# Kernel optimization log

Hardware: AMD Instinct MI355X
Metric: run time of the kernel (lower is better)

Reference implementation:

```python
import jax, jax.numpy as jnp
import numpy as np

B, IN_F, OUT_F, K = 8192, 1024, 4096, 2
S = 64  # sqrt(OUT_F)


def setup_inputs() -> dict:
    key = jax.random.key(0)
    k1, k2, k3, k4 = jax.random.split(key, 4)
    x = jax.random.normal(k1, (B, IN_F), dtype=jnp.float32)
    y = jax.random.normal(k2, (B, OUT_F), dtype=jnp.float32)
    weight = jax.random.normal(k3, (OUT_F, IN_F), dtype=jnp.float32) * (1.0 / np.sqrt(IN_F))
    bias = jax.random.normal(k4, (OUT_F,), dtype=jnp.float32) * (1.0 / np.sqrt(IN_F))
    return {"x": x, "y": y, "weight": weight, "bias": bias}


def reference(x, y, weight, bias):
    # fused GEMM + bias + residual add epilogue
    out_lin = jnp.einsum('bk,nk->bn', x, weight) + bias + y  # (B, OUT_F)
    feat = out_lin.reshape(B, S, S)
    # AvgPool2d(kernel=K, stride=K)
    s_out = S // K
    pooled = feat.reshape(B, s_out, K, s_out, K).mean(axis=(2, 4))  # (B, s_out, s_out)
    # divide by global mean of the pooled map
    mean_val = pooled.mean()
    normed = pooled / mean_val
    return normed[:, None, :, :]  # (B, 1, s_out, s_out)
```

## Files before the change

### kernel.cpp

```cpp
#include <hip/hip_runtime.h>
#include <stdint.h>


#define KDIM 1024
#define NP   1024
#define BM 128
#define BN 128
#define BK 64

typedef __bf16 bf16x8 __attribute__((ext_vector_type(8)));
typedef float f32x4 __attribute__((ext_vector_type(4)));

__device__ __forceinline__ unsigned f2bf(float f) {
  union { float f; unsigned u; } v; v.f = f;
  unsigned r = v.u + 0x7fffu + ((v.u >> 16) & 1u);
  return r >> 16;
}

__device__ __forceinline__ void gload_lds16(const void* g, void* l) {
  __builtin_amdgcn_global_load_lds(
      (const __attribute__((address_space(1))) void*)g,
      (__attribute__((address_space(3))) void*)l, 16, 0, 0);
}

__global__ void k_prep(const float* __restrict__ x, const float* __restrict__ W,
                       const float* __restrict__ bias,
                       unsigned short* __restrict__ xb, unsigned short* __restrict__ wp,
                       float* __restrict__ biasp) {
  int b = blockIdx.x;
  int t = threadIdx.x;
  if (b < 4096) {
    int i = b * 256 + t;
    const float4* x4 = (const float4*)x;
    float4 a = x4[i * 2], c = x4[i * 2 + 1];
    uint4 o;
    o.x = f2bf(a.x) | (f2bf(a.y) << 16);
    o.y = f2bf(a.z) | (f2bf(a.w) << 16);
    o.z = f2bf(c.x) | (f2bf(c.y) << 16);
    o.w = f2bf(c.z) | (f2bf(c.w) << 16);
    ((uint4*)xb)[i] = o;
  } else {
    int o = b - 4096;
    int r0 = ((o >> 5) << 7) + ((o & 31) << 1);
    const float4* W4 = (const float4*)W;
    float4 w0 = W4[(r0) * 256 + t];
    float4 w1 = W4[(r0 + 1) * 256 + t];
    float4 w2 = W4[(r0 + 64) * 256 + t];
    float4 w3 = W4[(r0 + 65) * 256 + t];
    float ax = 0.25f * (w0.x + w1.x + w2.x + w3.x);
    float ay = 0.25f * (w0.y + w1.y + w2.y + w3.y);
    float az = 0.25f * (w0.z + w1.z + w2.z + w3.z);
    float aw = 0.25f * (w0.w + w1.w + w2.w + w3.w);
    uint2 pk;
    pk.x = f2bf(ax) | (f2bf(ay) << 16);
    pk.y = f2bf(az) | (f2bf(aw) << 16);
    ((uint2*)wp)[o * 256 + t] = pk;
    if (t == 0)
      biasp[o] = 0.25f * (bias[r0] + bias[r0 + 1] + bias[r0 + 64] + bias[r0 + 65]);
  }
}

__global__ __launch_bounds__(256) void k_gemm(
    const unsigned short* __restrict__ xb, const unsigned short* __restrict__ wp,
    const float* __restrict__ biasp, const float* __restrict__ y,
    float* __restrict__ out, float* __restrict__ partials) {
  __shared__ char smem[65536];

  int bid = blockIdx.x;
  int wg = (bid & 7) * 64 + (bid >> 3);
  int bm0 = (wg >> 3) * BM;
  int bn0 = (wg & 7) * BN;

  int tid = threadIdx.x;
  int lane = tid & 63;
  int wid = tid >> 6;
  int wr = wid >> 1, wc = wid & 1;

  f32x4 acc[4][4];
#pragma unroll
  for (int i = 0; i < 4; i++)
#pragma unroll
    for (int j = 0; j < 4; j++) acc[i][j] = (f32x4)0.0f;

  int srow = wid * 32 + (lane >> 3);
  int scol = (((lane & 7) ^ (lane >> 3)) << 3);
  const unsigned short* aSrc = xb + (size_t)(bm0 + srow) * KDIM + scol;
  const unsigned short* bSrc = wp + (size_t)(bn0 + srow) * KDIM + scol;
  int ldsOff = wid * 4096;

  int rbase = (lane & 15) * 128;
  int xorv = (lane & 7) << 4;
  int cb0 = (((lane >> 4) * 16)) ^ xorv;
  int cb1 = ((64 + (lane >> 4) * 16)) ^ xorv;

#define STAGE(buf, ks)                                                         \
  {                                                                            \
    int k0 = (ks) * BK;                                                        \
    char* ab = smem + (buf) * 32768 + ldsOff;                                  \
    char* bb = smem + (buf) * 32768 + 16384 + ldsOff;                          \
    _Pragma("unroll")                                                          \
    for (int i = 0; i < 4; ++i) {                                              \
      gload_lds16(aSrc + (size_t)i * 8 * KDIM + k0, ab + i * 1024);            \
      gload_lds16(bSrc + (size_t)i * 8 * KDIM + k0, bb + i * 1024);            \
    }                                                                          \
  }

  STAGE(0, 0);
  for (int ks = 0; ks < 16; ++ks) {
    int cur = ks & 1;
    if (ks < 15) {
      STAGE(cur ^ 1, ks + 1);
      asm volatile("s_waitcnt vmcnt(8)" ::: "memory");
    } else {
      asm volatile("s_waitcnt vmcnt(0)" ::: "memory");
    }
    __builtin_amdgcn_s_barrier();
    asm volatile("" ::: "memory");
    const char* Ab = smem + cur * 32768;
    const char* Bb = Ab + 16384;
#pragma unroll
    for (int kk = 0; kk < 2; ++kk) {
      int cb = kk ? cb1 : cb0;
      bf16x8 af[4], bfr[4];
#pragma unroll
      for (int mi = 0; mi < 4; ++mi)
        af[mi] = *(const bf16x8*)(Ab + (wr * 64 + mi * 16) * 128 + rbase + cb);
#pragma unroll
      for (int ni = 0; ni < 4; ++ni)
        bfr[ni] = *(const bf16x8*)(Bb + (wc * 64 + ni * 16) * 128 + rbase + cb);
#pragma unroll
      for (int mi = 0; mi < 4; ++mi)
#pragma unroll
        for (int ni = 0; ni < 4; ++ni)
          acc[mi][ni] = __builtin_amdgcn_mfma_f32_16x16x32_bf16(af[mi], bfr[ni], acc[mi][ni], 0, 0, 0);
    }
    asm volatile("" ::: "memory");
    __builtin_amdgcn_s_barrier();
  }

  const float2* y2 = (const float2*)y;
  float tsum = 0.f;
  int r_l = (lane >> 4) * 4;
  int c_l = lane & 15;
#pragma unroll
  for (int mi = 0; mi < 4; ++mi) {
#pragma unroll
    for (int ni = 0; ni < 4; ++ni) {
      int col = bn0 + wc * 64 + ni * 16 + c_l;
      float bp = biasp[col];
      int y2base = ((col >> 5) << 6) + (col & 31);
#pragma unroll
      for (int j = 0; j < 4; ++j) {
        int row = bm0 + wr * 64 + mi * 16 + r_l + j;
        float2 u = y2[(size_t)row * 2048 + y2base];
        float2 v = y2[(size_t)row * 2048 + y2base + 32];
        float val = acc[mi][ni][j] + bp + 0.25f * (u.x + u.y + v.x + v.y);
        out[(size_t)row * NP + col] = val;
        tsum += val;
      }
    }
  }
#pragma unroll
  for (int off = 32; off > 0; off >>= 1) tsum += __shfl_down(tsum, off);
  float* ws4 = (float*)smem;
  __syncthreads();
  if (lane == 0) ws4[wid] = tsum;
  __syncthreads();
  if (tid == 0) partials[bid] = ws4[0] + ws4[1] + ws4[2] + ws4[3];
}

__global__ void k_reduce(const float* __restrict__ partials, float* __restrict__ invm) {
  __shared__ float s[256];
  int t = threadIdx.x;
  s[t] = partials[t] + partials[t + 256];
  __syncthreads();
  for (int off = 128; off > 0; off >>= 1) {
    if (t < off) s[t] += s[t + off];
    __syncthreads();
  }
  if (t == 0) invm[0] = 8388608.0f / s[0];
}

__global__ void k_norm(float* __restrict__ out, const float* __restrict__ invm) {
  int i = blockIdx.x * 256 + threadIdx.x;
  float inv = invm[0];
  float4* o4 = (float4*)out;
  float4 v = o4[i];
  v.x *= inv; v.y *= inv; v.z *= inv; v.w *= inv;
  o4[i] = v;
}

extern "C" void kernel_launch(void* const* d_in, const int* in_sizes, int n_in,
                              void* d_out, int out_size, void* d_ws, size_t ws_size,
                              hipStream_t stream) {
  (void)in_sizes; (void)n_in; (void)out_size; (void)ws_size;
  const float* x = (const float*)d_in[0];
  const float* y = (const float*)d_in[1];
  const float* W = (const float*)d_in[2];
  const float* bias = (const float*)d_in[3];
  float* out = (float*)d_out;

  char* ws = (char*)d_ws;
  unsigned short* xb = (unsigned short*)(ws);
  unsigned short* wp = (unsigned short*)(ws + 16777216);
  float* biasp = (float*)(ws + 16777216 + 2097152);
  float* partials = (float*)(ws + 16777216 + 2097152 + 4096);
  float* invm = (float*)(ws + 16777216 + 2097152 + 4096 + 2048);

  hipLaunchKernelGGL(k_prep, dim3(5120), dim3(256), 0, stream, x, W, bias, xb, wp, biasp);
  hipLaunchKernelGGL(k_gemm, dim3(512), dim3(256), 0, stream, xb, wp, biasp, y, out, partials);
  hipLaunchKernelGGL(k_reduce, dim3(1), dim3(256), 0, stream, partials, invm);
  hipLaunchKernelGGL(k_norm, dim3(8192), dim3(256), 0, stream, out, invm);
}
```

Baseline: 67.75 us.

## Split A/B staging around MFMA halves, prefetch epilogue loads, fuse reduce into norm

```diff
diff --git a/kernel.cpp b/kernel.cpp
--- a/kernel.cpp
+++ b/kernel.cpp
@@ -93,24 +93,30 @@
   int cb0 = (((lane >> 4) * 16)) ^ xorv;
   int cb1 = ((64 + (lane >> 4) * 16)) ^ xorv;
 
-#define STAGE(buf, ks)                                                         \
+#define STAGE_A(buf, ks)                                                       \
   {                                                                            \
     int k0 = (ks) * BK;                                                        \
     char* ab = smem + (buf) * 32768 + ldsOff;                                  \
+    _Pragma("unroll")                                                          \
+    for (int i = 0; i < 4; ++i)                                                \
+      gload_lds16(aSrc + (size_t)i * 8 * KDIM + k0, ab + i * 1024);            \
+  }
+#define STAGE_B(buf, ks)                                                       \
+  {                                                                            \
+    int k0 = (ks) * BK;                                                        \
     char* bb = smem + (buf) * 32768 + 16384 + ldsOff;                          \
     _Pragma("unroll")                                                          \
-    for (int i = 0; i < 4; ++i) {                                              \
-      gload_lds16(aSrc + (size_t)i * 8 * KDIM + k0, ab + i * 1024);            \
+    for (int i = 0; i < 4; ++i)                                                \
       gload_lds16(bSrc + (size_t)i * 8 * KDIM + k0, bb + i * 1024);            \
-    }                                                                          \
-  }
-
-  STAGE(0, 0);
+  }
+
+  STAGE_A(0, 0);
+  STAGE_B(0, 0);
   for (int ks = 0; ks < 16; ++ks) {
     int cur = ks & 1;
     if (ks < 15) {
-      STAGE(cur ^ 1, ks + 1);
-      asm volatile("s_waitcnt vmcnt(8)" ::: "memory");
+      STAGE_A(cur ^ 1, ks + 1);
+      asm volatile("s_waitcnt vmcnt(4)" ::: "memory");
     } else {
       asm volatile("s_waitcnt vmcnt(0)" ::: "memory");
     }
@@ -118,21 +124,38 @@
     asm volatile("" ::: "memory");
     const char* Ab = smem + cur * 32768;
     const char* Bb = Ab + 16384;
-#pragma unroll
-    for (int kk = 0; kk < 2; ++kk) {
-      int cb = kk ? cb1 : cb0;
+    {
       bf16x8 af[4], bfr[4];
 #pragma unroll
       for (int mi = 0; mi < 4; ++mi)
-        af[mi] = *(const bf16x8*)(Ab + (wr * 64 + mi * 16) * 128 + rbase + cb);
+        af[mi] = *(const bf16x8*)(Ab + (wr * 64 + mi * 16) * 128 + rbase + cb0);
 #pragma unroll
       for (int ni = 0; ni < 4; ++ni)
-        bfr[ni] = *(const bf16x8*)(Bb + (wc * 64 + ni * 16) * 128 + rbase + cb);
+        bfr[ni] = *(const bf16x8*)(Bb + (wc * 64 + ni * 16) * 128 + rbase + cb0);
+      __builtin_amdgcn_s_setprio(1);
 #pragma unroll
       for (int mi = 0; mi < 4; ++mi)
 #pragma unroll
         for (int ni = 0; ni < 4; ++ni)
           acc[mi][ni] = __builtin_amdgcn_mfma_f32_16x16x32_bf16(af[mi], bfr[ni], acc[mi][ni], 0, 0, 0);
+      __builtin_amdgcn_s_setprio(0);
+    }
+    if (ks < 15) STAGE_B(cur ^ 1, ks + 1);
+    {
+      bf16x8 af[4], bfr[4];
+#pragma unroll
+      for (int mi = 0; mi < 4; ++mi)
+        af[mi] = *(const bf16x8*)(Ab + (wr * 64 + mi * 16) * 128 + rbase + cb1);
+#pragma unroll
+      for (int ni = 0; ni < 4; ++ni)
+        bfr[ni] = *(const bf16x8*)(Bb + (wc * 64 + ni * 16) * 128 + rbase + cb1);
+      __builtin_amdgcn_s_setprio(1);
+#pragma unroll
+      for (int mi = 0; mi < 4; ++mi)
+#pragma unroll
+        for (int ni = 0; ni < 4; ++ni)
+          acc[mi][ni] = __builtin_amdgcn_mfma_f32_16x16x32_bf16(af[mi], bfr[ni], acc[mi][ni], 0, 0, 0);
+      __builtin_amdgcn_s_setprio(0);
     }
     asm volatile("" ::: "memory");
     __builtin_amdgcn_s_barrier();
@@ -142,48 +165,65 @@
   float tsum = 0.f;
   int r_l = (lane >> 4) * 4;
   int c_l = lane & 15;
-#pragma unroll
-  for (int mi = 0; mi < 4; ++mi) {
-#pragma unroll
-    for (int ni = 0; ni < 4; ++ni) {
-      int col = bn0 + wc * 64 + ni * 16 + c_l;
-      float bp = biasp[col];
-      int y2base = ((col >> 5) << 6) + (col & 31);
-#pragma unroll
-      for (int j = 0; j < 4; ++j) {
-        int row = bm0 + wr * 64 + mi * 16 + r_l + j;
-        float2 u = y2[(size_t)row * 2048 + y2base];
-        float2 v = y2[(size_t)row * 2048 + y2base + 32];
-        float val = acc[mi][ni][j] + bp + 0.25f * (u.x + u.y + v.x + v.y);
-        out[(size_t)row * NP + col] = val;
-        tsum += val;
-      }
-    }
-  }
+  float2 pu[2][4], pv[2][4];
+
+#define LOADG(buf, mi, ni)                                                     \
+  {                                                                            \
+    int col = bn0 + wc * 64 + (ni) * 16 + c_l;                                 \
+    int yb = ((col >> 5) << 6) + (col & 31);                                   \
+    _Pragma("unroll")                                                          \
+    for (int j = 0; j < 4; ++j) {                                              \
+      size_t row = (size_t)(bm0 + wr * 64 + (mi) * 16 + r_l + j);              \
+      pu[buf][j] = y2[row * 2048 + yb];                                        \
+      pv[buf][j] = y2[row * 2048 + yb + 32];                                   \
+    }                                                                          \
+  }
+#define CONS(buf, mi, ni)                                                      \
+  {                                                                            \
+    int col = bn0 + wc * 64 + (ni) * 16 + c_l;                                 \
+    float bp = biasp[col];                                                     \
+    _Pragma("unroll")                                                          \
+    for (int j = 0; j < 4; ++j) {                                              \
+      int row = bm0 + wr * 64 + (mi) * 16 + r_l + j;                           \
+      float val = acc[mi][ni][j] + bp +                                        \
+                  0.25f * (pu[buf][j].x + pu[buf][j].y + pv[buf][j].x + pv[buf][j].y); \
+      out[(size_t)row * NP + col] = val;                                       \
+      tsum += val;                                                             \
+    }                                                                          \
+  }
+
+  LOADG(0, 0, 0);
+#pragma unroll
+  for (int idx = 0; idx < 16; ++idx) {
+    int mi = idx >> 2, ni = idx & 3;
+    if (idx < 15) {
+      int mi2 = (idx + 1) >> 2, ni2 = (idx + 1) & 3;
+      LOADG((idx + 1) & 1, mi2, ni2);
+    }
+    CONS(idx & 1, mi, ni);
+  }
+
 #pragma unroll
   for (int off = 32; off > 0; off >>= 1) tsum += __shfl_down(tsum, off);
-  float* ws4 = (float*)smem;
+  float* sm = (float*)smem;
   __syncthreads();
-  if (lane == 0) ws4[wid] = tsum;
+  if (lane == 0) sm[wid] = tsum;
   __syncthreads();
-  if (tid == 0) partials[bid] = ws4[0] + ws4[1] + ws4[2] + ws4[3];
-}
-
-__global__ void k_reduce(const float* __restrict__ partials, float* __restrict__ invm) {
+  if (tid == 0) partials[bid] = (sm[0] + sm[1]) + (sm[2] + sm[3]);
+}
+
+__global__ void k_norm(float* __restrict__ out, const float* __restrict__ partials) {
   __shared__ float s[256];
   int t = threadIdx.x;
   s[t] = partials[t] + partials[t + 256];
   __syncthreads();
+#pragma unroll
   for (int off = 128; off > 0; off >>= 1) {
     if (t < off) s[t] += s[t + off];
     __syncthreads();
   }
-  if (t == 0) invm[0] = 8388608.0f / s[0];
-}
-
-__global__ void k_norm(float* __restrict__ out, const float* __restrict__ invm) {
-  int i = blockIdx.x * 256 + threadIdx.x;
-  float inv = invm[0];
+  float inv = 8388608.0f / s[0];
+  int i = blockIdx.x * 256 + t;
   float4* o4 = (float4*)out;
   float4 v = o4[i];
   v.x *= inv; v.y *= inv; v.z *= inv; v.w *= inv;
@@ -205,10 +245,8 @@
   unsigned short* wp = (unsigned short*)(ws + 16777216);
   float* biasp = (float*)(ws + 16777216 + 2097152);
   float* partials = (float*)(ws + 16777216 + 2097152 + 4096);
-  float* invm = (float*)(ws + 16777216 + 2097152 + 4096 + 2048);
 
   hipLaunchKernelGGL(k_prep, dim3(5120), dim3(256), 0, stream, x, W, bias, xb, wp, biasp);
   hipLaunchKernelGGL(k_gemm, dim3(512), dim3(256), 0, stream, xb, wp, biasp, y, out, partials);
-  hipLaunchKernelGGL(k_reduce, dim3(1), dim3(256), 0, stream, partials, invm);
-  hipLaunchKernelGGL(k_norm, dim3(8192), dim3(256), 0, stream, out, invm);
-}
+  hipLaunchKernelGGL(k_norm, dim3(8192), dim3(256), 0, stream, out, partials);
+}
```

Result: slower. 70.05 us (+3.4%).
